# Optimization experiments

Measured on AMD Instinct MI355X. Metric: run time of the kernel, lower is better.

## Reference

```python
import jax, jax.numpy as jnp
import numpy as np

# init constants: mul_vals=[1565,1342], shift_vals=[8,8]; module adds +7 to shifts
M0 = 1565
M1 = 1342
S0 = 8 + 7  # 15
S1 = 8 + 7  # 15


def _requant(x, m, s):
    # x * m, add rounding offset 1<<(s-1), truncate-to-int (torch LongTensor cast
    # truncates toward zero, matching astype on these positive-rounded values),
    # arithmetic right shift by s, clamp to [0, 255], back to float32.
    y = x * jnp.float32(m)
    y = (y + jnp.float32(1 << (s - 1))).astype(jnp.int64)
    y = jnp.right_shift(y, s).astype(jnp.float32)
    return jnp.clip(y, 0.0, 255.0)


def setup_inputs() -> dict:
    key = jax.random.key(0)
    k1, k2, k3, k4, k5 = jax.random.split(key, 5)
    B = 1048576
    X = jax.random.normal(k1, (B, 117), dtype=jnp.float32)
    W1 = jax.random.normal(k2, (20, 117), dtype=jnp.float32) * 0.1
    b1 = jax.random.normal(k3, (20,), dtype=jnp.float32) * 0.1
    W2 = jax.random.normal(k4, (2, 20), dtype=jnp.float32) * 0.1
    b2 = jax.random.normal(k5, (2,), dtype=jnp.float32) * 0.1
    return {"X": X, "W1": W1, "b1": b1, "W2": W2, "b2": b2}


def reference(X, W1, b1, W2, b2):
    # linear1: [B,117] @ [117,20] + b1
    h = jnp.einsum("bi,oi->bo", X, W1) + b1
    h = _requant(h, M0, S0)  # quantized ReLU-like clamp to [0,255]
    # linear2: [B,20] @ [20,2] + b2
    o = jnp.einsum("bi,oi->bo", h, W2) + b2
    o = _requant(o, M1, S1)
    return o
```

## Files before the change

### kernel.cpp

```cpp
#include <hip/hip_runtime.h>

#define COLS 117
#define NOUT1 20
#define ROWS 64
#define PSTR 21
#define PFROW (ROWS * PSTR)
#define PFSZ (4 * PFROW)

__device__ __forceinline__ float requant(float x, float m, float off, int s) {
  float y = __fmul_rn(x, m);
  y = __fadd_rn(y, off);
  long long yi = (long long)y;
  yi >>= s;
  float r = (float)yi;
  return fminf(fmaxf(r, 0.0f), 255.0f);
}

__global__ void transpose_w1(const float* __restrict__ W1, float* __restrict__ w1t) {
  for (int idx = threadIdx.x; idx < NOUT1 * COLS; idx += blockDim.x) {
    int o = idx / COLS, k = idx % COLS;
    w1t[k * NOUT1 + o] = W1[idx];
  }
}

template <bool TW>
__global__ __launch_bounds__(256, 5) void fann_kernel(
    const float* __restrict__ X, const float* __restrict__ W1,
    const float* __restrict__ b1, const float* __restrict__ W2,
    const float* __restrict__ b2, float* __restrict__ out) {
  __shared__ __align__(16) float xs[ROWS * COLS];
  float4* xs4 = (float4*)xs;
  const int t = threadIdx.x;
  {
    const float4* __restrict__ src =
        reinterpret_cast<const float4*>(X + (size_t)blockIdx.x * (ROWS * COLS));
    constexpr int NV = ROWS * COLS / 4;
    #pragma unroll
    for (int i = 0; i < NV / 256; ++i)
      xs4[t + i * 256] = src[t + i * 256];
    if (t < NV - (NV / 256) * 256)
      xs4[t + (NV / 256) * 256] = src[t + (NV / 256) * 256];
  }
  __syncthreads();

  const int w = __builtin_amdgcn_readfirstlane(t >> 6);
  const int l = t & 63;
  const int k0 = w * 29;
  const int kn = (w == 3) ? 30 : 29;

  float acc[NOUT1];
  #pragma unroll
  for (int o = 0; o < NOUT1; ++o) acc[o] = 0.0f;
  const float* xr = xs + l * COLS + k0;

  if (TW) {
    const float4* __restrict__ w4 =
        reinterpret_cast<const float4*>(W1) + (size_t)k0 * (NOUT1 / 4);
    for (int kk = 0; kk < kn; ++kk) {
      float x = xr[kk];
      #pragma unroll
      for (int j = 0; j < 5; ++j) {
        float4 wv = w4[kk * 5 + j];
        acc[4 * j + 0] = fmaf(x, wv.x, acc[4 * j + 0]);
        acc[4 * j + 1] = fmaf(x, wv.y, acc[4 * j + 1]);
        acc[4 * j + 2] = fmaf(x, wv.z, acc[4 * j + 2]);
        acc[4 * j + 3] = fmaf(x, wv.w, acc[4 * j + 3]);
      }
    }
  } else {
    for (int kk = 0; kk < kn; ++kk) {
      float x = xr[kk];
      #pragma unroll
      for (int o = 0; o < NOUT1; ++o)
        acc[o] = fmaf(x, W1[o * COLS + k0 + kk], acc[o]);
    }
  }

  __syncthreads();
  {
    float* pw = xs + w * PFROW + l * PSTR;
    #pragma unroll
    for (int o = 0; o < NOUT1; ++o) pw[o] = acc[o];
  }
  __syncthreads();

  float* sp0 = xs + PFSZ;
  float* sp1 = sp0 + 4 * 65;
  {
    float s0 = 0.0f, s1 = 0.0f;
    #pragma unroll
    for (int j = 0; j < 5; ++j) {
      const int o = w * 5 + j;
      float h = xs[0 * PFROW + l * PSTR + o] + xs[1 * PFROW + l * PSTR + o] +
                xs[2 * PFROW + l * PSTR + o] + xs[3 * PFROW + l * PSTR + o];
      h += b1[o];
      float hq = requant(h, 1565.0f, 16384.0f, 15);
      s0 = fmaf(hq, W2[o], s0);
      s1 = fmaf(hq, W2[NOUT1 + o], s1);
    }
    sp0[w * 65 + l] = s0;
    sp1[w * 65 + l] = s1;
  }
  __syncthreads();

  if (t < ROWS) {
    float s0 = sp0[t] + sp0[65 + t] + sp0[130 + t] + sp0[195 + t] + b2[0];
    float s1 = sp1[t] + sp1[65 + t] + sp1[130 + t] + sp1[195 + t] + b2[1];
    float2 r;
    r.x = requant(s0, 1342.0f, 16384.0f, 15);
    r.y = requant(s1, 1342.0f, 16384.0f, 15);
    reinterpret_cast<float2*>(out)[(size_t)blockIdx.x * ROWS + t] = r;
  }
}

__global__ void fann_tail(const float* __restrict__ X, const float* __restrict__ W1,
                          const float* __restrict__ b1, const float* __restrict__ W2,
                          const float* __restrict__ b2, float* __restrict__ out,
                          int start, int B) {
  int row = start + blockIdx.x * blockDim.x + threadIdx.x;
  if (row >= B) return;
  float acc[NOUT1];
  #pragma unroll
  for (int o = 0; o < NOUT1; ++o) acc[o] = b1[o];
  const float* xr = X + (size_t)row * COLS;
  for (int k = 0; k < COLS; ++k) {
    float x = xr[k];
    #pragma unroll
    for (int o = 0; o < NOUT1; ++o) acc[o] = fmaf(x, W1[o * COLS + k], acc[o]);
  }
  float s0 = b2[0], s1 = b2[1];
  #pragma unroll
  for (int o = 0; o < NOUT1; ++o) {
    float hq = requant(acc[o], 1565.0f, 16384.0f, 15);
    s0 = fmaf(hq, W2[o], s0);
    s1 = fmaf(hq, W2[NOUT1 + o], s1);
  }
  out[(size_t)row * 2 + 0] = requant(s0, 1342.0f, 16384.0f, 15);
  out[(size_t)row * 2 + 1] = requant(s1, 1342.0f, 16384.0f, 15);
}

extern "C" void kernel_launch(void* const* d_in, const int* in_sizes, int n_in,
                              void* d_out, int out_size, void* d_ws, size_t ws_size,
                              hipStream_t stream) {
  const float* X  = (const float*)d_in[0];
  const float* W1 = (const float*)d_in[1];
  const float* b1 = (const float*)d_in[2];
  const float* W2 = (const float*)d_in[3];
  const float* b2 = (const float*)d_in[4];
  float* out = (float*)d_out;
  const int B = in_sizes[0] / COLS;
  const int nblk = B / ROWS;
  const int tail = B - nblk * ROWS;

  const bool useT = ws_size >= (size_t)(COLS * NOUT1 * sizeof(float));
  if (useT) {
    float* w1t = (float*)d_ws;
    transpose_w1<<<1, 256, 0, stream>>>(W1, w1t);
    if (nblk > 0)
      fann_kernel<true><<<nblk, 256, 0, stream>>>(X, w1t, b1, W2, b2, out);
  } else {
    if (nblk > 0)
      fann_kernel<false><<<nblk, 256, 0, stream>>>(X, W1, b1, W2, b2, out);
  }
  if (tail > 0)
    fann_tail<<<(tail + 63) / 64, 64, 0, stream>>>(X, W1, b1, W2, b2, out,
                                                   nblk * ROWS, B);
}
```

Measured before the change: 108.1 us.

## Convert to persistent kernel with double-buffered register-staged tile prefetch

Replaces the one-block-per-tile launch with a persistent grid of 512 blocks that loop over tiles. Each block prefetches the next 64-row X tile into registers while computing the current tile from LDS, then writes it into a second LDS buffer. The goal is to hide global load latency behind compute. The cost is double the LDS (about 60 KB per block), which limits occupancy to about 2 blocks per CU, plus extra register pressure from the staged float4s.

Result: slower. 249.8 us (+131.1%).

```diff
diff --git a/kernel.cpp b/kernel.cpp
--- a/kernel.cpp
+++ b/kernel.cpp
@@ -3,9 +3,13 @@
 #define COLS 117
 #define NOUT1 20
 #define ROWS 64
+#define TILEF (ROWS * COLS)
+#define NV (TILEF / 4)
+#define REM (NV - 7 * 256)
 #define PSTR 21
 #define PFROW (ROWS * PSTR)
 #define PFSZ (4 * PFROW)
+#define GRID 512
 
 __device__ __forceinline__ float requant(float x, float m, float off, int s) {
   float y = __fmul_rn(x, m);
@@ -24,92 +28,115 @@
 }
 
 template <bool TW>
-__global__ __launch_bounds__(256, 5) void fann_kernel(
+__global__ __launch_bounds__(256, 2) void fann_persistent(
     const float* __restrict__ X, const float* __restrict__ W1,
     const float* __restrict__ b1, const float* __restrict__ W2,
-    const float* __restrict__ b2, float* __restrict__ out) {
-  __shared__ __align__(16) float xs[ROWS * COLS];
-  float4* xs4 = (float4*)xs;
-  const int t = threadIdx.x;
-  {
-    const float4* __restrict__ src =
-        reinterpret_cast<const float4*>(X + (size_t)blockIdx.x * (ROWS * COLS));
-    constexpr int NV = ROWS * COLS / 4;
+    const float* __restrict__ b2, float* __restrict__ out, int ntiles) {
+  __shared__ __align__(16) float buf[2][TILEF];
+  const int t256 = threadIdx.x;
+  const int w = __builtin_amdgcn_readfirstlane(t256 >> 6);
+  const int l = t256 & 63;
+  const int k0 = w * 29;
+  const int kn = (w == 3) ? 30 : 29;
+  const int G = gridDim.x;
+  const float4* __restrict__ Xv = reinterpret_cast<const float4*>(X);
+
+  int cur = 0;
+  int t = blockIdx.x;
+  if (t < ntiles) {
+    const float4* src = Xv + (size_t)t * NV;
+    float4 rr[8];
     #pragma unroll
-    for (int i = 0; i < NV / 256; ++i)
-      xs4[t + i * 256] = src[t + i * 256];
-    if (t < NV - (NV / 256) * 256)
-      xs4[t + (NV / 256) * 256] = src[t + (NV / 256) * 256];
+    for (int i = 0; i < 7; ++i) rr[i] = src[t256 + i * 256];
+    if (t256 < REM) rr[7] = src[t256 + 7 * 256];
+    float4* d = (float4*)buf[0];
+    #pragma unroll
+    for (int i = 0; i < 7; ++i) d[t256 + i * 256] = rr[i];
+    if (t256 < REM) d[t256 + 7 * 256] = rr[7];
   }
   __syncthreads();
 
-  const int w = __builtin_amdgcn_readfirstlane(t >> 6);
-  const int l = t & 63;
-  const int k0 = w * 29;
-  const int kn = (w == 3) ? 30 : 29;
+  for (; t < ntiles; t += G) {
+    const int tn = t + G;
+    const bool pf = (tn < ntiles);
+    float4 rr[8];
+    if (pf) {
+      const float4* src = Xv + (size_t)tn * NV;
+      #pragma unroll
+      for (int i = 0; i < 7; ++i) rr[i] = src[t256 + i * 256];
+      if (t256 < REM) rr[7] = src[t256 + 7 * 256];
+    }
 
-  float acc[NOUT1];
-  #pragma unroll
-  for (int o = 0; o < NOUT1; ++o) acc[o] = 0.0f;
-  const float* xr = xs + l * COLS + k0;
+    float acc[NOUT1];
+    #pragma unroll
+    for (int o = 0; o < NOUT1; ++o) acc[o] = 0.0f;
+    const float* xr = buf[cur] + l * COLS + k0;
+    if (TW) {
+      const float4* __restrict__ w4 =
+          reinterpret_cast<const float4*>(W1) + (size_t)k0 * (NOUT1 / 4);
+      for (int kk = 0; kk < kn; ++kk) {
+        float x = xr[kk];
+        #pragma unroll
+        for (int j = 0; j < 5; ++j) {
+          float4 wv = w4[kk * 5 + j];
+          acc[4 * j + 0] = fmaf(x, wv.x, acc[4 * j + 0]);
+          acc[4 * j + 1] = fmaf(x, wv.y, acc[4 * j + 1]);
+          acc[4 * j + 2] = fmaf(x, wv.z, acc[4 * j + 2]);
+          acc[4 * j + 3] = fmaf(x, wv.w, acc[4 * j + 3]);
+        }
+      }
+    } else {
+      for (int kk = 0; kk < kn; ++kk) {
+        float x = xr[kk];
+        #pragma unroll
+        for (int o = 0; o < NOUT1; ++o)
+          acc[o] = fmaf(x, W1[o * COLS + k0 + kk], acc[o]);
+      }
+    }
+    __syncthreads();
 
-  if (TW) {
-    const float4* __restrict__ w4 =
-        reinterpret_cast<const float4*>(W1) + (size_t)k0 * (NOUT1 / 4);
-    for (int kk = 0; kk < kn; ++kk) {
-      float x = xr[kk];
+    if (pf) {
+      float4* d = (float4*)buf[cur ^ 1];
+      #pragma unroll
+      for (int i = 0; i < 7; ++i) d[t256 + i * 256] = rr[i];
+      if (t256 < REM) d[t256 + 7 * 256] = rr[7];
+    }
+    float* scr = buf[cur];
+    {
+      float* pw = scr + w * PFROW + l * PSTR;
+      #pragma unroll
+      for (int o = 0; o < NOUT1; ++o) pw[o] = acc[o];
+    }
+    __syncthreads();
+
+    float* sp0 = scr + PFSZ;
+    float* sp1 = sp0 + 4 * 65;
+    {
+      float s0 = 0.0f, s1 = 0.0f;
       #pragma unroll
       for (int j = 0; j < 5; ++j) {
-        float4 wv = w4[kk * 5 + j];
-        acc[4 * j + 0] = fmaf(x, wv.x, acc[4 * j + 0]);
-        acc[4 * j + 1] = fmaf(x, wv.y, acc[4 * j + 1]);
-        acc[4 * j + 2] = fmaf(x, wv.z, acc[4 * j + 2]);
-        acc[4 * j + 3] = fmaf(x, wv.w, acc[4 * j + 3]);
+        const int o = w * 5 + j;
+        float h = scr[0 * PFROW + l * PSTR + o] + scr[1 * PFROW + l * PSTR + o] +
+                  scr[2 * PFROW + l * PSTR + o] + scr[3 * PFROW + l * PSTR + o];
+        h += b1[o];
+        float hq = requant(h, 1565.0f, 16384.0f, 15);
+        s0 = fmaf(hq, W2[o], s0);
+        s1 = fmaf(hq, W2[NOUT1 + o], s1);
       }
+      sp0[w * 65 + l] = s0;
+      sp1[w * 65 + l] = s1;
     }
-  } else {
-    for (int kk = 0; kk < kn; ++kk) {
-      float x = xr[kk];
-      #pragma unroll
-      for (int o = 0; o < NOUT1; ++o)
-        acc[o] = fmaf(x, W1[o * COLS + k0 + kk], acc[o]);
+    __syncthreads();
+
+    if (t256 < ROWS) {
+      float s0 = sp0[t256] + sp0[65 + t256] + sp0[130 + t256] + sp0[195 + t256] + b2[0];
+      float s1 = sp1[t256] + sp1[65 + t256] + sp1[130 + t256] + sp1[195 + t256] + b2[1];
+      float2 r;
+      r.x = requant(s0, 1342.0f, 16384.0f, 15);
+      r.y = requant(s1, 1342.0f, 16384.0f, 15);
+      reinterpret_cast<float2*>(out)[(size_t)t * ROWS + t256] = r;
     }
-  }
-
-  __syncthreads();
-  {
-    float* pw = xs + w * PFROW + l * PSTR;
-    #pragma unroll
-    for (int o = 0; o < NOUT1; ++o) pw[o] = acc[o];
-  }
-  __syncthreads();
-
-  float* sp0 = xs + PFSZ;
-  float* sp1 = sp0 + 4 * 65;
-  {
-    float s0 = 0.0f, s1 = 0.0f;
-    #pragma unroll
-    for (int j = 0; j < 5; ++j) {
-      const int o = w * 5 + j;
-      float h = xs[0 * PFROW + l * PSTR + o] + xs[1 * PFROW + l * PSTR + o] +
-                xs[2 * PFROW + l * PSTR + o] + xs[3 * PFROW + l * PSTR + o];
-      h += b1[o];
-      float hq = requant(h, 1565.0f, 16384.0f, 15);
-      s0 = fmaf(hq, W2[o], s0);
-      s1 = fmaf(hq, W2[NOUT1 + o], s1);
-    }
-    sp0[w * 65 + l] = s0;
-    sp1[w * 65 + l] = s1;
-  }
-  __syncthreads();
-
-  if (t < ROWS) {
-    float s0 = sp0[t] + sp0[65 + t] + sp0[130 + t] + sp0[195 + t] + b2[0];
-    float s1 = sp1[t] + sp1[65 + t] + sp1[130 + t] + sp1[195 + t] + b2[1];
-    float2 r;
-    r.x = requant(s0, 1342.0f, 16384.0f, 15);
-    r.y = requant(s1, 1342.0f, 16384.0f, 15);
-    reinterpret_cast<float2*>(out)[(size_t)blockIdx.x * ROWS + t] = r;
+    cur ^= 1;
   }
 }
 
@@ -149,20 +176,21 @@
   const float* b2 = (const float*)d_in[4];
   float* out = (float*)d_out;
   const int B = in_sizes[0] / COLS;
-  const int nblk = B / ROWS;
-  const int tail = B - nblk * ROWS;
+  const int ntiles = B / ROWS;
+  const int tail = B - ntiles * ROWS;
+  const int grid = (ntiles < GRID) ? (ntiles > 0 ? ntiles : 1) : GRID;
 
   const bool useT = ws_size >= (size_t)(COLS * NOUT1 * sizeof(float));
   if (useT) {
     float* w1t = (float*)d_ws;
     transpose_w1<<<1, 256, 0, stream>>>(W1, w1t);
-    if (nblk > 0)
-      fann_kernel<true><<<nblk, 256, 0, stream>>>(X, w1t, b1, W2, b2, out);
+    if (ntiles > 0)
+      fann_persistent<true><<<grid, 256, 0, stream>>>(X, w1t, b1, W2, b2, out, ntiles);
   } else {
-    if (nblk > 0)
-      fann_kernel<false><<<nblk, 256, 0, stream>>>(X, W1, b1, W2, b2, out);
+    if (ntiles > 0)
+      fann_persistent<false><<<grid, 256, 0, stream>>>(X, W1, b1, W2, b2, out, ntiles);
   }
   if (tail > 0)
     fann_tail<<<(tail + 63) / 64, 64, 0, stream>>>(X, W1, b1, W2, b2, out,
-                                                   nblk * ROWS, B);
+                                                   ntiles * ROWS, B);
 }
```

## Split K reduction across eight waves per block instead of four

Applied to the files above, without the earlier changes.

Doubles the block to 512 threads so eight waves each handle about 15 of the 117 input columns for the 64-row tile, instead of four waves handling 29. Partial sums are combined in shared memory in two phases: the first four waves write, then the other four accumulate. This shortens each thread's serial FMA chain and raises the number of waves per block to hide latency. In exchange it adds an extra barrier, read-modify-write shared-memory traffic, and a higher occupancy target (launch_bounds 8) that may constrain registers.

New measurement: 119.5 us. 10.6% more time.

```diff
diff --git a/kernel.cpp b/kernel.cpp
--- a/kernel.cpp
+++ b/kernel.cpp
@@ -3,9 +3,12 @@
 #define COLS 117
 #define NOUT1 20
 #define ROWS 64
+#define THREADS 512
+#define NV (ROWS * COLS / 4)
+#define FULLS (NV / THREADS)
+#define REMV (NV - FULLS * THREADS)
 #define PSTR 21
 #define PFROW (ROWS * PSTR)
-#define PFSZ (4 * PFROW)
 
 __device__ __forceinline__ float requant(float x, float m, float off, int s) {
   float y = __fmul_rn(x, m);
@@ -24,29 +27,26 @@
 }
 
 template <bool TW>
-__global__ __launch_bounds__(256, 5) void fann_kernel(
+__global__ __launch_bounds__(THREADS, 8) void fann_kernel(
     const float* __restrict__ X, const float* __restrict__ W1,
     const float* __restrict__ b1, const float* __restrict__ W2,
     const float* __restrict__ b2, float* __restrict__ out) {
   __shared__ __align__(16) float xs[ROWS * COLS];
   float4* xs4 = (float4*)xs;
-  const int t = threadIdx.x;
+  const int tid = threadIdx.x;
   {
     const float4* __restrict__ src =
-        reinterpret_cast<const float4*>(X + (size_t)blockIdx.x * (ROWS * COLS));
-    constexpr int NV = ROWS * COLS / 4;
+        reinterpret_cast<const float4*>(X) + (size_t)blockIdx.x * NV;
     #pragma unroll
-    for (int i = 0; i < NV / 256; ++i)
-      xs4[t + i * 256] = src[t + i * 256];
-    if (t < NV - (NV / 256) * 256)
-      xs4[t + (NV / 256) * 256] = src[t + (NV / 256) * 256];
+    for (int i = 0; i < FULLS; ++i) xs4[tid + i * THREADS] = src[tid + i * THREADS];
+    if (tid < REMV) xs4[tid + FULLS * THREADS] = src[tid + FULLS * THREADS];
   }
   __syncthreads();
 
-  const int w = __builtin_amdgcn_readfirstlane(t >> 6);
-  const int l = t & 63;
-  const int k0 = w * 29;
-  const int kn = (w == 3) ? 30 : 29;
+  const int w = __builtin_amdgcn_readfirstlane(tid >> 6);
+  const int l = tid & 63;
+  const int k0 = (w < 5) ? 15 * w : 75 + 14 * (w - 5);
+  const int kn = (w < 5) ? 15 : 14;
 
   float acc[NOUT1];
   #pragma unroll
@@ -75,18 +75,24 @@
         acc[o] = fmaf(x, W1[o * COLS + k0 + kk], acc[o]);
     }
   }
+  __syncthreads();
 
-  __syncthreads();
-  {
+  if (w < 4) {
     float* pw = xs + w * PFROW + l * PSTR;
     #pragma unroll
     for (int o = 0; o < NOUT1; ++o) pw[o] = acc[o];
   }
   __syncthreads();
+  if (w >= 4) {
+    float* pw = xs + (w - 4) * PFROW + l * PSTR;
+    #pragma unroll
+    for (int o = 0; o < NOUT1; ++o) pw[o] += acc[o];
+  }
+  __syncthreads();
 
-  float* sp0 = xs + PFSZ;
+  float* sp0 = xs + 4 * PFROW;
   float* sp1 = sp0 + 4 * 65;
-  {
+  if (w < 4) {
     float s0 = 0.0f, s1 = 0.0f;
     #pragma unroll
     for (int j = 0; j < 5; ++j) {
@@ -103,13 +109,13 @@
   }
   __syncthreads();
 
-  if (t < ROWS) {
-    float s0 = sp0[t] + sp0[65 + t] + sp0[130 + t] + sp0[195 + t] + b2[0];
-    float s1 = sp1[t] + sp1[65 + t] + sp1[130 + t] + sp1[195 + t] + b2[1];
+  if (tid < ROWS) {
+    float s0 = sp0[tid] + sp0[65 + tid] + sp0[130 + tid] + sp0[195 + tid] + b2[0];
+    float s1 = sp1[tid] + sp1[65 + tid] + sp1[130 + tid] + sp1[195 + tid] + b2[1];
     float2 r;
     r.x = requant(s0, 1342.0f, 16384.0f, 15);
     r.y = requant(s1, 1342.0f, 16384.0f, 15);
-    reinterpret_cast<float2*>(out)[(size_t)blockIdx.x * ROWS + t] = r;
+    reinterpret_cast<float2*>(out)[(size_t)blockIdx.x * ROWS + tid] = r;
   }
 }
 
@@ -157,10 +163,10 @@
     float* w1t = (float*)d_ws;
     transpose_w1<<<1, 256, 0, stream>>>(W1, w1t);
     if (nblk > 0)
-      fann_kernel<true><<<nblk, 256, 0, stream>>>(X, w1t, b1, W2, b2, out);
+      fann_kernel<true><<<nblk, THREADS, 0, stream>>>(X, w1t, b1, W2, b2, out);
   } else {
     if (nblk > 0)
-      fann_kernel<false><<<nblk, 256, 0, stream>>>(X, W1, b1, W2, b2, out);
+      fann_kernel<false><<<nblk, THREADS, 0, stream>>>(X, W1, b1, W2, b2, out);
   }
   if (tail > 0)
     fann_tail<<<(tail + 63) / 64, 64, 0, stream>>>(X, W1, b1, W2, b2, out,
```
